# Kernel tuning notes

Hardware: AMD Instinct MI355X
Metric: run time of the kernel (lower is better)

The kernel has to match this reference:

```python
import jax, jax.numpy as jnp
import numpy as np
import math

B, S, H = 8, 1024, 1024
LN_EPS = 1e-5  # assumed epsilon of create_normalization_layer('layer_norm')


def setup_inputs() -> dict:
    key = jax.random.key(0)
    ks = jax.random.split(key, 6)
    context = jax.random.normal(ks[0], (B, S, H), dtype=jnp.float32)
    mask = jnp.ones((B, 1, S), dtype=jnp.int32)
    prior = jax.random.uniform(ks[1], (B, S, S), dtype=jnp.float32)
    # LayerNorm params
    gamma = jnp.ones((H,), dtype=jnp.float32)
    beta = jnp.zeros((H,), dtype=jnp.float32)
    # Dense projections (Glorot-like init)
    scale = 1.0 / np.sqrt(H)
    Wk = jax.random.normal(ks[2], (H, H), dtype=jnp.float32) * scale
    bk = jnp.zeros((H,), dtype=jnp.float32)
    Wq = jax.random.normal(ks[3], (H, H), dtype=jnp.float32) * scale
    bq = jnp.zeros((H,), dtype=jnp.float32)
    return {"context": context, "mask": mask, "prior": prior,
            "gamma": gamma, "beta": beta, "Wk": Wk, "bk": bk, "Wq": Wq, "bq": bq}


def reference(context, mask, prior, gamma, beta, Wk, bk, Wq, bq):
    dtype = context.dtype
    s = context.shape[1]
    hs = context.shape[2]
    i = jnp.arange(s)
    adj_upper = i[:, None] == (i[None, :] - 1)          # [S,S] superdiagonal
    adj_lower = i[:, None] == (i[None, :] + 1)          # subdiagonal
    adj_mask = adj_upper | adj_lower
    pad = mask[:, 0, :].astype(bool)                    # [B,S]
    pad2d = pad[:, :, None] & pad[:, None, :]           # [B,S,S]
    final_adj = adj_mask[None, :, :] & pad2d

    # LayerNorm over last axis
    mu = jnp.mean(context, axis=-1, keepdims=True)
    var = jnp.mean(jnp.square(context - mu), axis=-1, keepdims=True)
    cn = (context - mu) * jax.lax.rsqrt(var + LN_EPS) * gamma + beta

    k = cn @ Wk + bk                                    # [B,S,H]
    q = cn @ Wq + bq
    scores = jnp.einsum('bsh,bth->bst', q, k) / math.sqrt(hs)
    scores = jnp.where(final_adj, scores, jnp.asarray(-1e9, dtype))
    neibor = jax.nn.softmax(scores, axis=-1)
    neibor = jnp.sqrt(neibor * jnp.swapaxes(neibor, 1, 2) + 1e-9)
    neibor = prior + (1.0 - prior) * neibor

    triu = i[None, :] >= i[:, None]                     # [S,S] upper incl diag
    tri = triu.astype(dtype)
    b_eye = jnp.eye(s, dtype=bool)

    t = jnp.log(neibor + 1e-9)
    t = jnp.where(adj_upper[None, :, :], t, jnp.asarray(0.0, dtype))
    t = jnp.einsum('bij,jk->bik', t, tri)               # cumulative over cols
    g = jnp.exp(jnp.einsum('ij,bjk->bik', tri, t))      # hierarchical prefix product
    keep = jnp.logical_not(jnp.logical_xor(triu, b_eye))
    g = jnp.where(keep[None, :, :], g, jnp.asarray(0.0, dtype))
    neibor_diag = jnp.where(b_eye[None, :, :], jnp.asarray(1e-9, dtype), neibor)
    g = g + jnp.swapaxes(g, 1, 2) + neibor_diag
    g = g / (jnp.sum(g, axis=-1, keepdims=True) + 1e-9)

    f2d = pad2d.astype(dtype)
    g = g * f2d
    neibor = neibor * f2d
    return g, neibor
```

## Files before the change

### kernel.cpp

```cpp
#include <hip/hip_runtime.h>
#include <hip/hip_bf16.h>

#define SB 8
#define SS 1024
#define SH 1024
#define LN_EPS 1e-5f

typedef unsigned short u16;
typedef __attribute__((ext_vector_type(8))) short bf16x8;
typedef __attribute__((ext_vector_type(4))) float f32x4;

__device__ __forceinline__ u16 f2bf(float f) {
  __hip_bfloat16 h = __float2bfloat16(f);
  return *reinterpret_cast<u16*>(&h);
}
__device__ __forceinline__ float bf2f(u16 x) {
  unsigned v = ((unsigned)x) << 16;
  return __builtin_bit_cast(float, v);
}

__device__ __forceinline__ void gld16(const void* g, void* l) {
  __builtin_amdgcn_global_load_lds(
      (const __attribute__((address_space(1))) void*)g,
      (__attribute__((address_space(3))) void*)l, 16, 0, 0);
}

__global__ __launch_bounds__(256) void prep(const float* __restrict__ x,
                                            const float* __restrict__ gamma,
                                            const float* __restrict__ beta,
                                            const float* __restrict__ Wq,
                                            const float* __restrict__ Wk,
                                            const float* __restrict__ bq,
                                            u16* __restrict__ cnb,
                                            u16* __restrict__ Wq_bf,
                                            u16* __restrict__ Wk_bf,
                                            float* __restrict__ wkbq,
                                            float* __restrict__ du,
                                            float* __restrict__ dd) {
  __shared__ float p1[4], p2[4];
  const int blk = blockIdx.x;
  const int t = threadIdx.x;
  const int wave = t >> 6, lane = t & 63;

  if (blk < SB * SS) {
    const float* xr = x + (size_t)blk * SH;
    float4 v = *(const float4*)(xr + 4 * t);

    float s = v.x + v.y + v.z + v.w;
#pragma unroll
    for (int off = 32; off > 0; off >>= 1) s += __shfl_down(s, off, 64);
    if (lane == 0) p1[wave] = s;
    __syncthreads();
    const float mu = (p1[0] + p1[1] + p1[2] + p1[3]) * (1.0f / SH);

    float d0 = v.x - mu, d1 = v.y - mu, d2 = v.z - mu, d3 = v.w - mu;
    float ss = d0 * d0 + d1 * d1 + d2 * d2 + d3 * d3;
#pragma unroll
    for (int off = 32; off > 0; off >>= 1) ss += __shfl_down(ss, off, 64);
    if (lane == 0) p2[wave] = ss;
    __syncthreads();
    const float rstd =
        rsqrtf((p2[0] + p2[1] + p2[2] + p2[3]) * (1.0f / SH) + LN_EPS);

    float4 gm = *(const float4*)(gamma + 4 * t);
    float4 bt = *(const float4*)(beta + 4 * t);
    ushort4 o;
    o.x = f2bf(d0 * rstd * gm.x + bt.x);
    o.y = f2bf(d1 * rstd * gm.y + bt.y);
    o.z = f2bf(d2 * rstd * gm.z + bt.z);
    o.w = f2bf(d3 * rstd * gm.w + bt.w);
    *(ushort4*)(cnb + (size_t)blk * SH + 4 * t) = o;
    if (t == 0) {
      du[blk] = 0.f;
      dd[blk] = 0.f;
    }
  } else {
    const int w = blk - SB * SS;
    const bool is_q = (w < SH);
    const float* src = is_q ? (Wq + (size_t)w * SH) : (Wk + (size_t)(w - SH) * SH);
    u16* dst = is_q ? (Wq_bf + (size_t)w * SH) : (Wk_bf + (size_t)(w - SH) * SH);
    float4 v = *(const float4*)(src + 4 * t);
    ushort4 o;
    o.x = f2bf(v.x); o.y = f2bf(v.y); o.z = f2bf(v.z); o.w = f2bf(v.w);
    *(ushort4*)(dst + 4 * t) = o;
    if (!is_q) {
      float4 b = *(const float4*)(bq + 4 * t);
      float s = v.x * b.x + v.y * b.y + v.z * b.z + v.w * b.w;
#pragma unroll
      for (int off = 32; off > 0; off >>= 1) s += __shfl_down(s, off, 64);
      if (lane == 0) p1[wave] = s;
      __syncthreads();
      if (t == 0) wkbq[w - SH] = p1[0] + p1[1] + p1[2] + p1[3];
    }
  }
}

#define BM 128
#define BN 128
#define BK 32
#define GK 1024
#define GN 1024

__global__ __launch_bounds__(256) void gemm_pt(const u16* __restrict__ A,
                                               const u16* __restrict__ Bt,
                                               u16* __restrict__ C) {
  __shared__ u16 As[BM * BK];
  __shared__ u16 Bs[BN * BK];
  const int tid = threadIdx.x;
  const int m0 = blockIdx.y * BM;
  const int n0 = blockIdx.x * BN;
  const int wave = tid >> 6, lane = tid & 63;
  const int wm = (wave & 1) * 64, wn = (wave >> 1) * 64;
  const int l15 = lane & 15, q = lane >> 4;

  f32x4 acc[4][4] = {};

  const int srow = tid >> 2;
  const int scol = 8 * (tid & 3);
  const u16* gA = A + (size_t)(m0 + srow) * GK + scol;
  const u16* gB = Bt + (size_t)(n0 + srow) * GK + scol;
  u16* lA = &As[srow * BK + scol];
  u16* lB = &Bs[srow * BK + scol];

  for (int k0 = 0; k0 < GK; k0 += BK) {
    __syncthreads();
    gld16(gA + k0, lA);
    gld16(gA + (size_t)64 * GK + k0, lA + 64 * BK);
    gld16(gB + k0, lB);
    gld16(gB + (size_t)64 * GK + k0, lB + 64 * BK);
    __syncthreads();

    bf16x8 af[4], bfr[4];
#pragma unroll
    for (int fm = 0; fm < 4; ++fm)
      af[fm] = *(const bf16x8*)&As[(wm + fm * 16 + l15) * BK + q * 8];
#pragma unroll
    for (int fn = 0; fn < 4; ++fn)
      bfr[fn] = *(const bf16x8*)&Bs[(wn + fn * 16 + l15) * BK + q * 8];
#pragma unroll
    for (int fm = 0; fm < 4; ++fm)
#pragma unroll
      for (int fn = 0; fn < 4; ++fn)
        acc[fm][fn] = __builtin_amdgcn_mfma_f32_16x16x32_bf16(
            af[fm], bfr[fn], acc[fm][fn], 0, 0, 0);
  }

#pragma unroll
  for (int fm = 0; fm < 4; ++fm)
#pragma unroll
    for (int fn = 0; fn < 4; ++fn) {
      const int row0 = m0 + wm + fm * 16 + q * 4;
      const int col = n0 + wn + fn * 16 + l15;
#pragma unroll
      for (int r = 0; r < 4; ++r)
        C[(size_t)(row0 + r) * GN + col] = f2bf(acc[fm][fn][r]);
    }
}

__global__ __launch_bounds__(256) void ugemm_fused(const u16* __restrict__ A,
                                                   const u16* __restrict__ Bt,
                                                   const u16* __restrict__ cnb,
                                                   const float* __restrict__ wkbq,
                                                   float* __restrict__ du,
                                                   float* __restrict__ dd) {
  __shared__ u16 As[BM * BK];
  __shared__ u16 Bs[BN * BK];
  const int tid = threadIdx.x;
  const int m0 = blockIdx.y * BM;
  const int n0 = blockIdx.x * BN;
  const int wave = tid >> 6, lane = tid & 63;
  const int wm = (wave & 1) * 64, wn = (wave >> 1) * 64;
  const int l15 = lane & 15, q = lane >> 4;

  f32x4 acc[4][4] = {};

  const int srow = tid >> 2;
  const int scol = 8 * (tid & 3);
  const u16* gA = A + (size_t)(m0 + srow) * GK + scol;
  const u16* gB = Bt + (size_t)(n0 + srow) * GK + scol;
  u16* lA = &As[srow * BK + scol];
  u16* lB = &Bs[srow * BK + scol];

  for (int k0 = 0; k0 < GK; k0 += BK) {
    __syncthreads();
    gld16(gA + k0, lA);
    gld16(gA + (size_t)64 * GK + k0, lA + 64 * BK);
    gld16(gB + k0, lB);
    gld16(gB + (size_t)64 * GK + k0, lB + 64 * BK);
    __syncthreads();

    bf16x8 af[4], bfr[4];
#pragma unroll
    for (int fm = 0; fm < 4; ++fm)
      af[fm] = *(const bf16x8*)&As[(wm + fm * 16 + l15) * BK + q * 8];
#pragma unroll
    for (int fn = 0; fn < 4; ++fn)
      bfr[fn] = *(const bf16x8*)&Bs[(wn + fn * 16 + l15) * BK + q * 8];
#pragma unroll
    for (int fm = 0; fm < 4; ++fm)
#pragma unroll
      for (int fn = 0; fn < 4; ++fn)
        acc[fm][fn] = __builtin_amdgcn_mfma_f32_16x16x32_bf16(
            af[fm], bfr[fn], acc[fm][fn], 0, 0, 0);
  }

  float wb[4];
#pragma unroll
  for (int fn = 0; fn < 4; ++fn) wb[fn] = wkbq[n0 + wn + fn * 16 + l15];

#pragma unroll
  for (int fm = 0; fm < 4; ++fm) {
#pragma unroll
    for (int rr = 0; rr < 4; ++rr) {
      const int r = m0 + wm + fm * 16 + q * 4 + rr;
      const int sl = r & (SS - 1);
      float sdu = 0.f, sdd = 0.f;
#pragma unroll
      for (int fn = 0; fn < 4; ++fn) {
        const int col = n0 + wn + fn * 16 + l15;
        const float a = acc[fm][fn][rr] + wb[fn];
        if (sl < SS - 1) sdu += a * bf2f(cnb[(size_t)(r + 1) * SH + col]);
        if (sl > 0)      sdd += a * bf2f(cnb[(size_t)(r - 1) * SH + col]);
      }
#pragma unroll
      for (int m = 1; m < 16; m <<= 1) {
        sdu += __shfl_xor(sdu, m, 64);
        sdd += __shfl_xor(sdd, m, 64);
      }
      if (l15 == 0) {
        atomicAdd(&du[r], sdu);
        atomicAdd(&dd[r], sdd);
      }
    }
  }
}

__device__ __forceinline__ void soft2(const float* __restrict__ du,
                                      const float* __restrict__ dd, int x,
                                      float& pu, float& pd) {
  const int sl = x & (SS - 1);
  if (sl == 0) { pu = 1.f; pd = 0.f; }
  else if (sl == SS - 1) { pu = 0.f; pd = 1.f; }
  else {
    const float a = du[x] * 0.03125f;
    const float b = dd[x] * 0.03125f;
    const float m = fmaxf(a, b);
    const float eu = __expf(a - m), ed = __expf(b - m);
    const float inv = 1.f / (eu + ed);
    pu = eu * inv;
    pd = ed * inv;
  }
}

__global__ __launch_bounds__(256) void rows_fused(const float* __restrict__ prior,
                                                  const int* __restrict__ mask,
                                                  const float* __restrict__ du,
                                                  const float* __restrict__ dd,
                                                  float* __restrict__ g_out,
                                                  float* __restrict__ ne_out) {
  const int r = blockIdx.x;
  const int b = r >> 10, i = r & (SS - 1);
  const int t = threadIdx.x;
  const int wave = t >> 6, lane = t & 63;
  const float nbz = 3.1622776601683795e-5f;

  float nb_im1 = nbz, nb_ip1 = nbz;
  if (i >= 1) {
    float pu_m, pd_m, pu_c, pd_c;
    soft2(du, dd, r - 1, pu_m, pd_m);
    soft2(du, dd, r, pu_c, pd_c);
    nb_im1 = sqrtf(pu_m * pd_c + 1e-9f);
  }
  if (i <= SS - 2) {
    float pu_c, pd_c, pu_p, pd_p;
    soft2(du, dd, r, pu_c, pd_c);
    soft2(du, dd, r + 1, pu_p, pd_p);
    nb_ip1 = sqrtf(pu_c * pd_p + 1e-9f);
  }

  const float* prow = prior + (size_t)r * SS;
  float4 pr = *(const float4*)(prow + 4 * t);
  const int* mrow = mask + b * SS;
  const float padi = (mrow[i] != 0) ? 1.f : 0.f;
  int4 mk = *(const int4*)(mrow + 4 * t);

  float ne[4], gsum = 0.f;
#pragma unroll
  for (int v = 0; v < 4; ++v) {
    const int k = 4 * t + v;
    const float p = (&pr.x)[v];
    const float nb = (k == i - 1) ? nb_im1 : (k == i + 1) ? nb_ip1 : nbz;
    const float n = p + (1.f - p) * nb;
    ne[v] = n;
    gsum += (k == i) ? (2.f + 1e-9f) : (1.f + n);
  }

  __shared__ float part[4];
#pragma unroll
  for (int off = 32; off > 0; off >>= 1) gsum += __shfl_down(gsum, off, 64);
  if (lane == 0) part[wave] = gsum;
  __syncthreads();
  const float inv = 1.f / (part[0] + part[1] + part[2] + part[3] + 1e-9f);

  float4 go, no;
#pragma unroll
  for (int v = 0; v < 4; ++v) {
    const int k = 4 * t + v;
    const float padk = ((&mk.x)[v] != 0) ? 1.f : 0.f;
    const float f2 = padi * padk;
    const float gt = (k == i) ? (2.f + 1e-9f) : (1.f + ne[v]);
    (&go.x)[v] = gt * inv * f2;
    (&no.x)[v] = ne[v] * f2;
  }
  *(float4*)(g_out + (size_t)r * SS + 4 * t) = go;
  *(float4*)(ne_out + (size_t)r * SS + 4 * t) = no;
}

extern "C" void kernel_launch(void* const* d_in, const int* in_sizes, int n_in,
                              void* d_out, int out_size, void* d_ws, size_t ws_size,
                              hipStream_t stream) {
  const float* context = (const float*)d_in[0];
  const int* mask = (const int*)d_in[1];
  const float* prior = (const float*)d_in[2];
  const float* gamma = (const float*)d_in[3];
  const float* beta = (const float*)d_in[4];
  const float* Wk = (const float*)d_in[5];
  const float* bk = (const float*)d_in[6];
  const float* Wq = (const float*)d_in[7];
  const float* bq = (const float*)d_in[8];
  (void)bk;

  float* out_g = (float*)d_out;
  float* out_n = out_g + (size_t)SB * SS * SS;

  char* ws = (char*)d_ws;
  u16* cnb = (u16*)ws;
  u16* Wq_bf = (u16*)(ws + ((size_t)16 << 20));
  u16* Wk_bf = (u16*)(ws + ((size_t)18 << 20));
  u16* PT = (u16*)(ws + ((size_t)20 << 20));
  float* wkbq = (float*)(ws + ((size_t)22 << 20));
  float* du = (float*)(ws + ((size_t)23 << 20));
  float* dd = (float*)(ws + ((size_t)24 << 20));

  prep<<<SB * SS + 2 * SH / 1, 256, 0, stream>>>(context, gamma, beta, Wq, Wk,
                                                 bq, cnb, Wq_bf, Wk_bf, wkbq,
                                                 du, dd);
  gemm_pt<<<dim3(8, 8), 256, 0, stream>>>(Wk_bf, Wq_bf, PT);
  ugemm_fused<<<dim3(8, 64), 256, 0, stream>>>(cnb, PT, cnb, wkbq, du, dd);
  rows_fused<<<SB * SS, 256, 0, stream>>>(prior, mask, du, dd, out_g, out_n);
}
```

Before: 196.5 us.

## Shrink weight GEMM tiles and split main GEMM along K for more blocks

After: 205.3 us. +4.5%, slower.

```diff
diff --git a/kernel.cpp b/kernel.cpp
--- a/kernel.cpp
+++ b/kernel.cpp
@@ -95,67 +95,61 @@
   }
 }
 
-#define BM 128
-#define BN 128
-#define BK 32
 #define GK 1024
 #define GN 1024
 
-__global__ __launch_bounds__(256) void gemm_pt(const u16* __restrict__ A,
-                                               const u16* __restrict__ Bt,
-                                               u16* __restrict__ C) {
-  __shared__ u16 As[BM * BK];
-  __shared__ u16 Bs[BN * BK];
+__global__ __launch_bounds__(256) void gemm_pt64(const u16* __restrict__ A,
+                                                 const u16* __restrict__ Bt,
+                                                 u16* __restrict__ C) {
+  __shared__ u16 As[64 * 32];
+  __shared__ u16 Bs[64 * 32];
   const int tid = threadIdx.x;
-  const int m0 = blockIdx.y * BM;
-  const int n0 = blockIdx.x * BN;
+  const int m0 = blockIdx.y * 64;
+  const int n0 = blockIdx.x * 64;
   const int wave = tid >> 6, lane = tid & 63;
-  const int wm = (wave & 1) * 64, wn = (wave >> 1) * 64;
+  const int wn = wave * 16;
   const int l15 = lane & 15, q = lane >> 4;
 
-  f32x4 acc[4][4] = {};
+  f32x4 acc[4] = {};
 
   const int srow = tid >> 2;
   const int scol = 8 * (tid & 3);
   const u16* gA = A + (size_t)(m0 + srow) * GK + scol;
   const u16* gB = Bt + (size_t)(n0 + srow) * GK + scol;
-  u16* lA = &As[srow * BK + scol];
-  u16* lB = &Bs[srow * BK + scol];
-
-  for (int k0 = 0; k0 < GK; k0 += BK) {
+  u16* lA = &As[srow * 32 + scol];
+  u16* lB = &Bs[srow * 32 + scol];
+
+  for (int k0 = 0; k0 < GK; k0 += 32) {
     __syncthreads();
     gld16(gA + k0, lA);
-    gld16(gA + (size_t)64 * GK + k0, lA + 64 * BK);
     gld16(gB + k0, lB);
-    gld16(gB + (size_t)64 * GK + k0, lB + 64 * BK);
-    __syncthreads();
-
-    bf16x8 af[4], bfr[4];
+    __syncthreads();
+
+    bf16x8 af[4];
 #pragma unroll
     for (int fm = 0; fm < 4; ++fm)
-      af[fm] = *(const bf16x8*)&As[(wm + fm * 16 + l15) * BK + q * 8];
-#pragma unroll
-    for (int fn = 0; fn < 4; ++fn)
-      bfr[fn] = *(const bf16x8*)&Bs[(wn + fn * 16 + l15) * BK + q * 8];
+      af[fm] = *(const bf16x8*)&As[(fm * 16 + l15) * 32 + q * 8];
+    bf16x8 bfr = *(const bf16x8*)&Bs[(wn + l15) * 32 + q * 8];
 #pragma unroll
     for (int fm = 0; fm < 4; ++fm)
-#pragma unroll
-      for (int fn = 0; fn < 4; ++fn)
-        acc[fm][fn] = __builtin_amdgcn_mfma_f32_16x16x32_bf16(
-            af[fm], bfr[fn], acc[fm][fn], 0, 0, 0);
-  }
-
-#pragma unroll
-  for (int fm = 0; fm < 4; ++fm)
-#pragma unroll
-    for (int fn = 0; fn < 4; ++fn) {
-      const int row0 = m0 + wm + fm * 16 + q * 4;
-      const int col = n0 + wn + fn * 16 + l15;
-#pragma unroll
-      for (int r = 0; r < 4; ++r)
-        C[(size_t)(row0 + r) * GN + col] = f2bf(acc[fm][fn][r]);
-    }
-}
+      acc[fm] = __builtin_amdgcn_mfma_f32_16x16x32_bf16(af[fm], bfr, acc[fm],
+                                                        0, 0, 0);
+  }
+
+#pragma unroll
+  for (int fm = 0; fm < 4; ++fm) {
+    const int row0 = m0 + fm * 16 + q * 4;
+    const int col = n0 + wn + l15;
+#pragma unroll
+    for (int r = 0; r < 4; ++r)
+      C[(size_t)(row0 + r) * GN + col] = f2bf(acc[fm][r]);
+  }
+}
+
+#define BM 128
+#define BN 128
+#define BK 32
+#define KSPLIT 512
 
 __global__ __launch_bounds__(256) void ugemm_fused(const u16* __restrict__ A,
                                                    const u16* __restrict__ Bt,
@@ -168,6 +162,7 @@
   const int tid = threadIdx.x;
   const int m0 = blockIdx.y * BM;
   const int n0 = blockIdx.x * BN;
+  const int kbase = blockIdx.z * KSPLIT;
   const int wave = tid >> 6, lane = tid & 63;
   const int wm = (wave & 1) * 64, wn = (wave >> 1) * 64;
   const int l15 = lane & 15, q = lane >> 4;
@@ -176,12 +171,12 @@
 
   const int srow = tid >> 2;
   const int scol = 8 * (tid & 3);
-  const u16* gA = A + (size_t)(m0 + srow) * GK + scol;
-  const u16* gB = Bt + (size_t)(n0 + srow) * GK + scol;
+  const u16* gA = A + (size_t)(m0 + srow) * GK + kbase + scol;
+  const u16* gB = Bt + (size_t)(n0 + srow) * GK + kbase + scol;
   u16* lA = &As[srow * BK + scol];
   u16* lB = &Bs[srow * BK + scol];
 
-  for (int k0 = 0; k0 < GK; k0 += BK) {
+  for (int k0 = 0; k0 < KSPLIT; k0 += BK) {
     __syncthreads();
     gld16(gA + k0, lA);
     gld16(gA + (size_t)64 * GK + k0, lA + 64 * BK);
@@ -205,8 +200,10 @@
   }
 
   float wb[4];
-#pragma unroll
-  for (int fn = 0; fn < 4; ++fn) wb[fn] = wkbq[n0 + wn + fn * 16 + l15];
+  const float wgate = (blockIdx.z == 0) ? 1.f : 0.f;
+#pragma unroll
+  for (int fn = 0; fn < 4; ++fn)
+    wb[fn] = wgate * wkbq[n0 + wn + fn * 16 + l15];
 
 #pragma unroll
   for (int fm = 0; fm < 4; ++fm) {
@@ -342,10 +339,9 @@
   float* du = (float*)(ws + ((size_t)23 << 20));
   float* dd = (float*)(ws + ((size_t)24 << 20));
 
-  prep<<<SB * SS + 2 * SH / 1, 256, 0, stream>>>(context, gamma, beta, Wq, Wk,
-                                                 bq, cnb, Wq_bf, Wk_bf, wkbq,
-                                                 du, dd);
-  gemm_pt<<<dim3(8, 8), 256, 0, stream>>>(Wk_bf, Wq_bf, PT);
-  ugemm_fused<<<dim3(8, 64), 256, 0, stream>>>(cnb, PT, cnb, wkbq, du, dd);
+  prep<<<SB * SS + 2 * SH, 256, 0, stream>>>(context, gamma, beta, Wq, Wk, bq,
+                                             cnb, Wq_bf, Wk_bf, wkbq, du, dd);
+  gemm_pt64<<<dim3(16, 16), 256, 0, stream>>>(Wk_bf, Wq_bf, PT);
+  ugemm_fused<<<dim3(8, 64, 2), 256, 0, stream>>>(cnb, PT, cnb, wkbq, du, dd);
   rows_fused<<<SB * SS, 256, 0, stream>>>(prior, mask, du, dd, out_g, out_n);
 }
```
